# Kernel tuning notes

Measured on AMD Instinct MI355X. Metric: run time of the kernel, lower is better.

The kernel has to match this reference:

```python
import jax, jax.numpy as jnp
import numpy as np

B, S, D = 32, 8192, 64


def setup_inputs() -> dict:
    key = jax.random.key(0)
    k1, k2 = jax.random.split(key)
    input_real = jax.random.normal(k1, (B, S, D), dtype=jnp.float32)
    input_imag = jax.random.normal(k2, (B, S, D), dtype=jnp.float32)
    return {"input_real": input_real, "input_imag": input_imag}


def reference(input_real, input_imag):
    # ComplexMixture: mean over seq of per-token complex outer products v v^H.
    # Original builds [B,S,D,D] via 4 batch_dots then means over S; fused here
    # as Gram contractions over the sequence axis (no [B,S,D,D] intermediate).
    seq_len = input_real.shape[1]
    inv_s = jnp.asarray(1.0 / seq_len, dtype=input_real.dtype)
    rr = jnp.einsum('bsi,bsj->bij', input_real, input_real)
    ii = jnp.einsum('bsi,bsj->bij', input_imag, input_imag)
    ri = jnp.einsum('bsi,bsj->bij', input_real, input_imag)
    out_real = (rr + ii) * inv_s                     # [B, D, D], symmetric
    out_imag = (ri - jnp.swapaxes(ri, 1, 2)) * inv_s  # [B, D, D], antisymmetric
    return (out_real, out_imag)
```

## Files before the change

### kernel.cpp

```cpp
#include <hip/hip_runtime.h>


#define BATCH 32
#define SEQ   8192
#define DD    64
#define CHUNKS 16
#define SCHUNK (SEQ / CHUNKS)
#define BK     128
#define NIT    (SCHUNK / BK)

typedef __bf16 bf16x8 __attribute__((ext_vector_type(8)));
typedef float  f32x16 __attribute__((ext_vector_type(16)));

__device__ __forceinline__ unsigned bf16pk(float a, float b) {
  unsigned ua = __builtin_bit_cast(unsigned, a);
  unsigned ub = __builtin_bit_cast(unsigned, b);
  ua = (ua + 0x7fffu + ((ua >> 16) & 1u)) >> 16;
  ub = (ub + 0x7fffu + ((ub >> 16) & 1u)) >> 16;
  return (ua & 0xffffu) | (ub << 16);
}

__global__ __launch_bounds__(256, 2) void gram_partial(
    const float* __restrict__ R, const float* __restrict__ I,
    float* __restrict__ ws)
{
  __shared__ uint4 lds[32][64];
  const int tid  = threadIdx.x;
  const int wave = tid >> 6;
  const int lane = tid & 63;
  const int b = blockIdx.x & 31;
  const int c = blockIdx.x >> 5;
  const float* Rb = R + (size_t)b * (SEQ * DD);
  const float* Ib = I + (size_t)b * (SEQ * DD);
  const int m0 = (wave >> 1) * 32;
  const int n0 = (wave & 1) * 32;
  const int l31 = lane & 31;
  const int lhi = lane >> 5;

  f32x16 accR = {};
  f32x16 accI = {};

  const int chunk0 = c * SCHUNK;

  for (int it = 0; it < NIT; ++it) {
    const int sbase = chunk0 + it * BK;
    #pragma unroll
    for (int gi = 0; gi < 4; ++gi) {
      const int g = gi * 4 + wave;
      const float* pR = Rb + (size_t)(sbase + g * 8) * DD + lane;
      const float* pI = Ib + (size_t)(sbase + g * 8) * DD + lane;
      float r0 = pR[0*64], r1 = pR[1*64], r2 = pR[2*64], r3 = pR[3*64];
      float r4 = pR[4*64], r5 = pR[5*64], r6 = pR[6*64], r7 = pR[7*64];
      float i0 = pI[0*64], i1 = pI[1*64], i2 = pI[2*64], i3 = pI[3*64];
      float i4 = pI[4*64], i5 = pI[5*64], i6 = pI[6*64], i7 = pI[7*64];
      uint4 qR; qR.x = bf16pk(r0, r1); qR.y = bf16pk(r2, r3);
                qR.z = bf16pk(r4, r5); qR.w = bf16pk(r6, r7);
      uint4 qI; qI.x = bf16pk(i0, i1); qI.y = bf16pk(i2, i3);
                qI.z = bf16pk(i4, i5); qI.w = bf16pk(i6, i7);
      lds[g][lane]      = qR;
      lds[16 + g][lane] = qI;
    }
    __syncthreads();
    #pragma unroll
    for (int ks = 0; ks < BK / 16; ++ks) {
      const int kg = ks * 2 + lhi;
      bf16x8 aR = __builtin_bit_cast(bf16x8, lds[kg][m0 + l31]);
      bf16x8 bR = __builtin_bit_cast(bf16x8, lds[kg][n0 + l31]);
      bf16x8 aI = __builtin_bit_cast(bf16x8, lds[16 + kg][m0 + l31]);
      bf16x8 bI = __builtin_bit_cast(bf16x8, lds[16 + kg][n0 + l31]);
      accR = __builtin_amdgcn_mfma_f32_32x32x16_bf16(aR, bR, accR, 0, 0, 0);
      accR = __builtin_amdgcn_mfma_f32_32x32x16_bf16(aI, bI, accR, 0, 0, 0);
      accI = __builtin_amdgcn_mfma_f32_32x32x16_bf16(aR, bI, accI, 0, 0, 0);
    }
    __syncthreads();
  }

  float* wsR = ws + ((size_t)(c * 32 + b) * 2) * 4096;
  float* wsM = wsR + 4096;
  const int jj = n0 + l31;
  #pragma unroll
  for (int r = 0; r < 16; ++r) {
    const int i = m0 + (r & 3) + 8 * (r >> 2) + 4 * lhi;
    wsR[i * 64 + jj] = accR[r];
  }
  float* ldsf = (float*)lds;
  #pragma unroll
  for (int r = 0; r < 16; ++r) {
    const int i = m0 + (r & 3) + 8 * (r >> 2) + 4 * lhi;
    ldsf[i * 65 + jj] = accI[r];
  }
  __syncthreads();
  #pragma unroll
  for (int k = 0; k < 16; ++k) {
    const int e = tid + 256 * k;
    const int i = e >> 6, j = e & 63;
    wsM[e] = ldsf[i * 65 + j] - ldsf[j * 65 + i];
  }
}

__global__ __launch_bounds__(256) void gram_reduce(
    const float* __restrict__ ws, float* __restrict__ out)
{
  const int gtid = blockIdx.x * 256 + threadIdx.x;
  const float inv = 1.0f / (float)SEQ;
  #pragma unroll
  for (int k = 0; k < 4; ++k) {
    const int o    = gtid + k * 65536;
    const int kind = o >> 17;
    const int rem  = o & 131071;
    const int b    = rem >> 12;
    const int e    = rem & 4095;
    float s = 0.0f;
    #pragma unroll
    for (int c = 0; c < CHUNKS; ++c)
      s += ws[((size_t)(c * 32 + b) * 2 + kind) * 4096 + e];
    out[o] = s * inv;
  }
}

extern "C" void kernel_launch(void* const* d_in, const int* in_sizes, int n_in,
                              void* d_out, int out_size, void* d_ws, size_t ws_size,
                              hipStream_t stream) {
  const float* R = (const float*)d_in[0];
  const float* I = (const float*)d_in[1];
  float* out = (float*)d_out;
  float* ws  = (float*)d_ws;

  gram_partial<<<BATCH * CHUNKS, 256, 0, stream>>>(R, I, ws);
  gram_reduce<<<256, 256, 0, stream>>>(ws, out);
}
```

Measured before the change: 168.0 us.

## Template chunk count, raise occupancy, batch loads, vectorize reduce

The sequence split becomes a template parameter, and 32 chunks are used when the workspace is large enough, which doubles the partial-Gram grid to 1024 blocks. Launch bounds rise to 4 blocks per CU, and all 64 global loads per iteration are issued before any bf16 packing to increase memory-level parallelism. The reduce kernel now uses float4 loads and stores. The costs are higher register pressure, twice the workspace traffic in the reduce, and a larger partial-sum buffer.

```diff
diff --git a/kernel.cpp b/kernel.cpp
--- a/kernel.cpp
+++ b/kernel.cpp
@@ -4,10 +4,7 @@
 #define BATCH 32
 #define SEQ   8192
 #define DD    64
-#define CHUNKS 16
-#define SCHUNK (SEQ / CHUNKS)
-#define BK     128
-#define NIT    (SCHUNK / BK)
+#define BK    128
 
 typedef __bf16 bf16x8 __attribute__((ext_vector_type(8)));
 typedef float  f32x16 __attribute__((ext_vector_type(16)));
@@ -20,10 +17,13 @@
   return (ua & 0xffffu) | (ub << 16);
 }
 
-__global__ __launch_bounds__(256, 2) void gram_partial(
+template<int CHUNKS>
+__global__ __launch_bounds__(256, 4) void gram_partial(
     const float* __restrict__ R, const float* __restrict__ I,
     float* __restrict__ ws)
 {
+  constexpr int SCHUNK = SEQ / CHUNKS;
+  constexpr int NIT    = SCHUNK / BK;
   __shared__ uint4 lds[32][64];
   const int tid  = threadIdx.x;
   const int wave = tid >> 6;
@@ -44,19 +44,22 @@
 
   for (int it = 0; it < NIT; ++it) {
     const int sbase = chunk0 + it * BK;
+    float rv[4][8], iv[4][8];
     #pragma unroll
     for (int gi = 0; gi < 4; ++gi) {
       const int g = gi * 4 + wave;
       const float* pR = Rb + (size_t)(sbase + g * 8) * DD + lane;
       const float* pI = Ib + (size_t)(sbase + g * 8) * DD + lane;
-      float r0 = pR[0*64], r1 = pR[1*64], r2 = pR[2*64], r3 = pR[3*64];
-      float r4 = pR[4*64], r5 = pR[5*64], r6 = pR[6*64], r7 = pR[7*64];
-      float i0 = pI[0*64], i1 = pI[1*64], i2 = pI[2*64], i3 = pI[3*64];
-      float i4 = pI[4*64], i5 = pI[5*64], i6 = pI[6*64], i7 = pI[7*64];
-      uint4 qR; qR.x = bf16pk(r0, r1); qR.y = bf16pk(r2, r3);
-                qR.z = bf16pk(r4, r5); qR.w = bf16pk(r6, r7);
-      uint4 qI; qI.x = bf16pk(i0, i1); qI.y = bf16pk(i2, i3);
-                qI.z = bf16pk(i4, i5); qI.w = bf16pk(i6, i7);
+      #pragma unroll
+      for (int j = 0; j < 8; ++j) { rv[gi][j] = pR[j * 64]; iv[gi][j] = pI[j * 64]; }
+    }
+    #pragma unroll
+    for (int gi = 0; gi < 4; ++gi) {
+      const int g = gi * 4 + wave;
+      uint4 qR; qR.x = bf16pk(rv[gi][0], rv[gi][1]); qR.y = bf16pk(rv[gi][2], rv[gi][3]);
+                qR.z = bf16pk(rv[gi][4], rv[gi][5]); qR.w = bf16pk(rv[gi][6], rv[gi][7]);
+      uint4 qI; qI.x = bf16pk(iv[gi][0], iv[gi][1]); qI.y = bf16pk(iv[gi][2], iv[gi][3]);
+                qI.z = bf16pk(iv[gi][4], iv[gi][5]); qI.w = bf16pk(iv[gi][6], iv[gi][7]);
       lds[g][lane]      = qR;
       lds[16 + g][lane] = qI;
     }
@@ -98,24 +101,24 @@
   }
 }
 
+template<int CHUNKS>
 __global__ __launch_bounds__(256) void gram_reduce(
-    const float* __restrict__ ws, float* __restrict__ out)
+    const float4* __restrict__ ws, float4* __restrict__ out)
 {
-  const int gtid = blockIdx.x * 256 + threadIdx.x;
+  const int o = blockIdx.x * 256 + threadIdx.x;
+  const int kind = o >> 15;
+  const int rem  = o & 32767;
+  const int b    = rem >> 10;
+  const int e    = rem & 1023;
   const float inv = 1.0f / (float)SEQ;
+  float sx = 0.f, sy = 0.f, sz = 0.f, sw = 0.f;
   #pragma unroll
-  for (int k = 0; k < 4; ++k) {
-    const int o    = gtid + k * 65536;
-    const int kind = o >> 17;
-    const int rem  = o & 131071;
-    const int b    = rem >> 12;
-    const int e    = rem & 4095;
-    float s = 0.0f;
-    #pragma unroll
-    for (int c = 0; c < CHUNKS; ++c)
-      s += ws[((size_t)(c * 32 + b) * 2 + kind) * 4096 + e];
-    out[o] = s * inv;
+  for (int c = 0; c < CHUNKS; ++c) {
+    float4 v = ws[((size_t)(c * 32 + b) * 2 + kind) * 1024 + e];
+    sx += v.x; sy += v.y; sz += v.z; sw += v.w;
   }
+  float4 r; r.x = sx * inv; r.y = sy * inv; r.z = sz * inv; r.w = sw * inv;
+  out[o] = r;
 }
 
 extern "C" void kernel_launch(void* const* d_in, const int* in_sizes, int n_in,
@@ -126,6 +129,12 @@
   float* out = (float*)d_out;
   float* ws  = (float*)d_ws;
 
-  gram_partial<<<BATCH * CHUNKS, 256, 0, stream>>>(R, I, ws);
-  gram_reduce<<<256, 256, 0, stream>>>(ws, out);
+  const size_t need32 = (size_t)32 * 32 * 2 * 4096 * 4;
+  if (ws_size >= need32) {
+    gram_partial<32><<<BATCH * 32, 256, 0, stream>>>(R, I, ws);
+    gram_reduce<32><<<256, 256, 0, stream>>>((const float4*)ws, (float4*)out);
+  } else {
+    gram_partial<16><<<BATCH * 16, 256, 0, stream>>>(R, I, ws);
+    gram_reduce<16><<<256, 256, 0, stream>>>((const float4*)ws, (float4*)out);
+  }
 }
```

Measured after the change: 161.6 us. 3.8% less time.
